# Kernel optimization log

Measured on AMD Instinct MI355X. Metric: run time of the kernel, lower is better.

Reference implementation:

```python
import jax, jax.numpy as jnp
import numpy as np

B = 64        # batch
V1 = 4096     # nodes, layer 1 (D)
V2 = 1024     # nodes after pool/4
DF = 8        # input features (DFeat)
K1 = 25       # Chebyshev order layer 1
K2 = 25       # Chebyshev order layer 2
F1 = 32       # CL1_F
F2 = 64       # CL2_F
FC1F = 512    # FC1_F
FC2F = 10     # FC2_F
E1 = 65536    # nnz of L1
E2 = 16384    # nnz of L2
FC1Fin = F2 * (V1 // 16)  # 16384


def setup_inputs() -> dict:
    key = jax.random.key(0)
    ks = jax.random.split(key, 16)
    x = jax.random.normal(ks[0], (B, V1, DF), jnp.float32)
    L1_rows = jax.random.randint(ks[1], (E1,), 0, V1, dtype=jnp.int32)
    L1_cols = jax.random.randint(ks[2], (E1,), 0, V1, dtype=jnp.int32)
    # small values keep the order-25 Chebyshev recursion numerically tame
    L1_vals = jax.random.normal(ks[3], (E1,), jnp.float32) * 0.05
    L2_rows = jax.random.randint(ks[4], (E2,), 0, V2, dtype=jnp.int32)
    L2_cols = jax.random.randint(ks[5], (E2,), 0, V2, dtype=jnp.int32)
    L2_vals = jax.random.normal(ks[6], (E2,), jnp.float32) * 0.05

    def glorot(k, shape, fin, fout):
        s = np.sqrt(2.0 / (fin + fout)).astype(np.float32)
        return jax.random.uniform(k, shape, jnp.float32, -s, s)

    cl1_w = glorot(ks[7], (F1, K1 * DF), K1, F1)
    cl1_b = jnp.zeros((F1,), jnp.float32)
    cl2_w = glorot(ks[8], (F2, K2 * F1), K2 * F1, F2)
    cl2_b = jnp.zeros((F2,), jnp.float32)
    fc1_w = glorot(ks[9], (FC1F, FC1Fin), FC1Fin, FC1F)
    fc1_b = jnp.zeros((FC1F,), jnp.float32)
    fc2_w = glorot(ks[10], (FC2F, FC1F), FC1F, FC2F)
    fc2_b = jnp.zeros((FC2F,), jnp.float32)
    return dict(x=x, L1_rows=L1_rows, L1_cols=L1_cols, L1_vals=L1_vals,
                L2_rows=L2_rows, L2_cols=L2_cols, L2_vals=L2_vals,
                cl1_w=cl1_w, cl1_b=cl1_b, cl2_w=cl2_w, cl2_b=cl2_b,
                fc1_w=fc1_w, fc1_b=fc1_b, fc2_w=fc2_w, fc2_b=fc2_b)


def _cheb_conv(x, rows, cols, vals, W, b, K):
    """Chebyshev graph conv. x: [B, V, Fin]; sparse L as COO edge lists."""
    Bb, V, Fin = x.shape
    x0 = x.transpose(1, 2, 0).reshape(V, Fin * Bb)  # [V, Fin*B]

    def spmm(y):  # sparse [V,V] @ dense [V, C]
        return jax.ops.segment_sum(vals[:, None] * y[cols], rows, num_segments=V)

    x1 = spmm(x0)

    def step(carry, _):
        xm2, xm1 = carry
        xk = 2.0 * spmm(xm1) - xm2
        return (xm1, xk), xk

    _, rest = jax.lax.scan(step, (x0, x1), None, length=K - 2)
    stack = jnp.concatenate([x0[None], x1[None], rest], axis=0)  # [K, V, Fin*B]
    # [K,V,Fin,B] -> [B,V,Fin,K] -> [B*V, Fin*K], matching torch layout
    feat = stack.reshape(K, V, Fin, Bb).transpose(3, 1, 2, 0).reshape(Bb * V, Fin * K)
    out = feat @ W.T + b
    return out.reshape(Bb, V, -1)


def _max_pool(x, p):
    Bb, V, F = x.shape
    return x.reshape(Bb, V // p, p, F).max(axis=2)


def reference(x, L1_rows, L1_cols, L1_vals, L2_rows, L2_cols, L2_vals,
              cl1_w, cl1_b, cl2_w, cl2_b, fc1_w, fc1_b, fc2_w, fc2_b):
    h = _cheb_conv(x, L1_rows, L1_cols, L1_vals, cl1_w, cl1_b, K1)
    h = jax.nn.relu(h)
    h = _max_pool(h, 4)                                   # [B, V/4, F1]
    h = _cheb_conv(h, L2_rows, L2_cols, L2_vals, cl2_w, cl2_b, K2)
    h = jax.nn.relu(h)
    h = _max_pool(h, 4)                                   # [B, V/16, F2]
    h = h.reshape(-1, FC1Fin)
    h = jax.nn.relu(h @ fc1_w.T + fc1_b)
    # dropout treated as identity (eval mode / d=0)
    return h @ fc2_w.T + fc2_b                            # [B, FC2F]
```

## Files before the change

kernel.cpp:

```cpp
#include <hip/hip_runtime.h>
#include <hip/hip_fp16.h>

#define B_    64
#define V1_   4096
#define V2_   1024
#define DF_   8
#define K_    25
#define NP_   13
#define F1_   32
#define F2_   64
#define FC1F_ 512
#define FC2F_ 10
#define E1_   65536
#define E2_   16384
#define C1_   512
#define C2_   2048
#define FCIN_ 16384

typedef short bf16x8 __attribute__((ext_vector_type(8)));
typedef float f32x4  __attribute__((ext_vector_type(4)));

#define FMA_MIX_LO(acc, qv, gv) \
    asm("v_fma_mix_f32 %0, %1, %2, %0 op_sel:[1,0,0] op_sel_hi:[1,1,0]" \
        : "+v"(acc) : "v"(qv), "v"(gv))
#define FMA_MIX_HI(acc, qv, gv) \
    asm("v_fma_mix_f32 %0, %1, %2, %0 op_sel:[1,1,0] op_sel_hi:[1,1,0]" \
        : "+v"(acc) : "v"(qv), "v"(gv))

__device__ __forceinline__ unsigned short f2bf(float x) {
    unsigned u = __float_as_uint(x);
    u += 0x7FFFu + ((u >> 16) & 1u);
    return (unsigned short)(u >> 16);
}
__device__ __forceinline__ float h2f_lo(unsigned u) {
    return __half2float(__ushort_as_half((unsigned short)(u & 0xFFFFu)));
}
__device__ __forceinline__ float h2f_hi(unsigned u) {
    return __half2float(__ushort_as_half((unsigned short)(u >> 16)));
}

__global__ __launch_bounds__(256) void k_transpose_rm(const float* __restrict__ x,
                                                      unsigned* __restrict__ XP,
                                                      unsigned* __restrict__ stk0) {
    __shared__ float tsh[DF_][B_][16];
    const int t = threadIdx.x;
    const int v0 = blockIdx.x * 16;
    for (int rep = 0; rep < 4; ++rep) {
        int idx = rep*256 + t;
        int b = idx >> 4, vv = idx & 15;
        const float4* p = (const float4*)&x[((size_t)b*V1_ + v0 + vv)*DF_];
        float4 a0 = p[0], a1 = p[1];
        tsh[0][b][vv]=a0.x; tsh[1][b][vv]=a0.y; tsh[2][b][vv]=a0.z; tsh[3][b][vv]=a0.w;
        tsh[4][b][vv]=a1.x; tsh[5][b][vv]=a1.y; tsh[6][b][vv]=a1.z; tsh[7][b][vv]=a1.w;
    }
    __syncthreads();
    for (int rep = 0; rep < 16; ++rep) {
        int idx = rep*256 + t;
        int c2 = idx & 255, vv = idx >> 8;
        int c = c2*2, fin = c >> 6, b = c & 63;
        float xa = tsh[fin][b][vv], xb = tsh[fin][b+1][vv];
        __half2 hh = __floats2half2_rn(xa, xb);
        XP[(size_t)(v0+vv)*256 + c2]   = *(const unsigned*)&hh;
        stk0[(size_t)(v0+vv)*256 + c2] = (unsigned)f2bf(xa) | ((unsigned)f2bf(xb) << 16);
    }
}

__global__ __launch_bounds__(256) void k_count(const int* __restrict__ rows, int E,
                                               int* __restrict__ cnt) {
    int e = blockIdx.x*256 + threadIdx.x;
    if (e < E) atomicAdd(&cnt[rows[e]], 1);
}

__global__ __launch_bounds__(256) void k_scan(const int* __restrict__ cnt, int V,
                                              int* __restrict__ offs, int* __restrict__ cursor) {
    __shared__ int psum[256];
    int t = threadIdx.x;
    int chunk = V >> 8;
    int lo = t*chunk;
    int s = 0;
    for (int i = lo; i < lo+chunk; ++i) s += (cnt[i] + 3) & ~3;
    psum[t] = s;
    __syncthreads();
    for (int off = 1; off < 256; off <<= 1) {
        int val = (t >= off) ? psum[t-off] : 0;
        __syncthreads();
        psum[t] += val;
        __syncthreads();
    }
    int run = (t == 0) ? 0 : psum[t-1];
    for (int i = lo; i < lo+chunk; ++i) {
        offs[i] = run; cursor[i] = run;
        run += (cnt[i] + 3) & ~3;
    }
    if (t == 255) offs[V] = run;
}

__global__ __launch_bounds__(256) void k_scatter(const int* __restrict__ rows,
                                                 const int* __restrict__ cols,
                                                 const float* __restrict__ vals, int E,
                                                 int shift,
                                                 int* __restrict__ cursor,
                                                 unsigned* __restrict__ ep) {
    int e = blockIdx.x*256 + threadIdx.x;
    if (e < E) {
        int p = atomicAdd(&cursor[rows[e]], 1);
        unsigned hv = (unsigned)__half_as_ushort(__float2half(vals[e]));
        ep[p] = (hv << 16) | ((unsigned)cols[e] << shift);
    }
}

__global__ __launch_bounds__(512) void k_dcheb1(int k,
        const unsigned short* __restrict__ Xsrc,
        unsigned short* __restrict__ Xown,
        unsigned short* __restrict__ stk16,
        const int* __restrict__ offs,
        const unsigned* __restrict__ ep) {
    const int t = threadIdx.x;
    const int lane = t & 63;
    const int v = blockIdx.x*8 + (t >> 6);
    const int e0 = offs[v], e1 = offs[v+1];
    const unsigned loff = (unsigned)lane * 16u;
    float acc[8];
#pragma unroll
    for (int j = 0; j < 8; ++j) acc[j] = 0.f;
    const char* srcb = (const char*)Xsrc;

    for (int e = e0; e < e1; e += 4) {
        const uint4 q = *(const uint4*)&ep[e];
        const uint4 g0 = *(const uint4*)(srcb + ((q.x & 0xFFFFu)*1024u + loff));
        const uint4 g1 = *(const uint4*)(srcb + ((q.y & 0xFFFFu)*1024u + loff));
        const uint4 g2 = *(const uint4*)(srcb + ((q.z & 0xFFFFu)*1024u + loff));
        const uint4 g3 = *(const uint4*)(srcb + ((q.w & 0xFFFFu)*1024u + loff));
        FMA_MIX_LO(acc[0], q.x, g0.x); FMA_MIX_HI(acc[1], q.x, g0.x);
        FMA_MIX_LO(acc[2], q.x, g0.y); FMA_MIX_HI(acc[3], q.x, g0.y);
        FMA_MIX_LO(acc[4], q.x, g0.z); FMA_MIX_HI(acc[5], q.x, g0.z);
        FMA_MIX_LO(acc[6], q.x, g0.w); FMA_MIX_HI(acc[7], q.x, g0.w);
        FMA_MIX_LO(acc[0], q.y, g1.x); FMA_MIX_HI(acc[1], q.y, g1.x);
        FMA_MIX_LO(acc[2], q.y, g1.y); FMA_MIX_HI(acc[3], q.y, g1.y);
        FMA_MIX_LO(acc[4], q.y, g1.z); FMA_MIX_HI(acc[5], q.y, g1.z);
        FMA_MIX_LO(acc[6], q.y, g1.w); FMA_MIX_HI(acc[7], q.y, g1.w);
        FMA_MIX_LO(acc[0], q.z, g2.x); FMA_MIX_HI(acc[1], q.z, g2.x);
        FMA_MIX_LO(acc[2], q.z, g2.y); FMA_MIX_HI(acc[3], q.z, g2.y);
        FMA_MIX_LO(acc[4], q.z, g2.z); FMA_MIX_HI(acc[5], q.z, g2.z);
        FMA_MIX_LO(acc[6], q.z, g2.w); FMA_MIX_HI(acc[7], q.z, g2.w);
        FMA_MIX_LO(acc[0], q.w, g3.x); FMA_MIX_HI(acc[1], q.w, g3.x);
        FMA_MIX_LO(acc[2], q.w, g3.y); FMA_MIX_HI(acc[3], q.w, g3.y);
        FMA_MIX_LO(acc[4], q.w, g3.z); FMA_MIX_HI(acc[5], q.w, g3.z);
        FMA_MIX_LO(acc[6], q.w, g3.w); FMA_MIX_HI(acc[7], q.w, g3.w);
    }

    float xn[8];
    if (k > 1) {
        const uint4 old = *(const uint4*)((const char*)Xown + ((size_t)v*1024 + loff));
        xn[0] = fmaf(2.f, acc[0], -h2f_lo(old.x));
        xn[1] = fmaf(2.f, acc[1], -h2f_hi(old.x));
        xn[2] = fmaf(2.f, acc[2], -h2f_lo(old.y));
        xn[3] = fmaf(2.f, acc[3], -h2f_hi(old.y));
        xn[4] = fmaf(2.f, acc[4], -h2f_lo(old.z));
        xn[5] = fmaf(2.f, acc[5], -h2f_hi(old.z));
        xn[6] = fmaf(2.f, acc[6], -h2f_lo(old.w));
        xn[7] = fmaf(2.f, acc[7], -h2f_hi(old.w));
    } else {
#pragma unroll
        for (int j = 0; j < 8; ++j) xn[j] = acc[j];
    }

    uint4 hp;
    { __half2 h0 = __floats2half2_rn(xn[0], xn[1]); hp.x = *(const unsigned*)&h0;
      __half2 h1 = __floats2half2_rn(xn[2], xn[3]); hp.y = *(const unsigned*)&h1;
      __half2 h2 = __floats2half2_rn(xn[4], xn[5]); hp.z = *(const unsigned*)&h2;
      __half2 h3 = __floats2half2_rn(xn[6], xn[7]); hp.w = *(const unsigned*)&h3; }
    *(uint4*)((char*)Xown + ((size_t)v*1024 + loff)) = hp;

    uint4 bp;
    bp.x = (unsigned)f2bf(xn[0]) | ((unsigned)f2bf(xn[1]) << 16);
    bp.y = (unsigned)f2bf(xn[2]) | ((unsigned)f2bf(xn[3]) << 16);
    bp.z = (unsigned)f2bf(xn[4]) | ((unsigned)f2bf(xn[5]) << 16);
    bp.w = (unsigned)f2bf(xn[6]) | ((unsigned)f2bf(xn[7]) << 16);
    *(uint4*)((char*)stk16 + (((size_t)k*V1_ + v)*1024 + loff)) = bp;
}

template<int FIN, int F>
__global__ __launch_bounds__(256) void k_wprep(const float* __restrict__ W,
                                               unsigned short* __restrict__ Wb) {
    int idx = blockIdx.x*256 + threadIdx.x;
    int kk  = idx & 7;
    int f   = (idx >> 3) % F;
    int g   = (idx >> 3) / F % 4;
    int fin = idx / (8*F*4);
    int k = g*8 + kk;
    Wb[idx] = (k < K_) ? f2bf(W[(size_t)f*(FIN*K_) + fin*K_ + k]) : 0;
}

__global__ __launch_bounds__(256) void k_wprep_fc(const float* __restrict__ W,
                                                  unsigned short* __restrict__ Wb) {
    int idx = (blockIdx.x*256 + threadIdx.x)*4;
    float4 w = *(const float4*)&W[idx];
    ushort4 o;
    o.x = f2bf(w.x); o.y = f2bf(w.y); o.z = f2bf(w.z); o.w = f2bf(w.w);
    *(ushort4*)&Wb[idx] = o;
}

__global__ __launch_bounds__(256) void k_gemm1b(const unsigned short* __restrict__ stk16,
                                                const unsigned short* __restrict__ Wb,
                                                const float* __restrict__ bias,
                                                float* __restrict__ X0T2) {
    const int t = threadIdx.x, lane = t & 63, wave = t >> 6;
    const int v2 = blockIdx.x*4 + wave;
    const int m = lane & 15, g = lane >> 4;
    int kbase[8];
#pragma unroll
    for (int j = 0; j < 8; ++j) {
        int kq = g*8 + j; if (kq > 24) kq = 24;
        kbase[j] = kq * (V1_*C1_);
    }
    float bv[2] = { bias[m], bias[16+m] };
    f32x4 pool[4][2];

    for (int vv = 0; vv < 4; ++vv) {
        const int v = v2*4 + vv;
        f32x4 acc[4][2];
#pragma unroll
        for (int mt = 0; mt < 4; ++mt)
#pragma unroll
            for (int ft = 0; ft < 2; ++ft) acc[mt][ft] = (f32x4){0.f,0.f,0.f,0.f};

        for (int fin = 0; fin < DF_; ++fin) {
            const int cbase = v*C1_ + fin*64 + m;
            const bf16x8 bw0 = *(const bf16x8*)&Wb[((fin*4+g)*F1_ + m)*8];
            const bf16x8 bw1 = *(const bf16x8*)&Wb[((fin*4+g)*F1_ + 16 + m)*8];
#pragma unroll
            for (int mt = 0; mt < 4; ++mt) {
                unsigned short au[8];
#pragma unroll
                for (int j = 0; j < 8; ++j)
                    au[j] = stk16[(size_t)(kbase[j] + cbase + mt*16)];
                bf16x8 a;
                __builtin_memcpy(&a, au, 16);
                acc[mt][0] = __builtin_amdgcn_mfma_f32_16x16x32_bf16(a, bw0, acc[mt][0], 0,0,0);
                acc[mt][1] = __builtin_amdgcn_mfma_f32_16x16x32_bf16(a, bw1, acc[mt][1], 0,0,0);
            }
        }
#pragma unroll
        for (int mt = 0; mt < 4; ++mt)
#pragma unroll
            for (int ft = 0; ft < 2; ++ft) {
                if (vv == 0) pool[mt][ft] = acc[mt][ft];
                else {
#pragma unroll
                    for (int j = 0; j < 4; ++j)
                        pool[mt][ft][j] = fmaxf(pool[mt][ft][j], acc[mt][ft][j]);
                }
            }
    }

#pragma unroll
    for (int mt = 0; mt < 4; ++mt)
#pragma unroll
        for (int ft = 0; ft < 2; ++ft)
#pragma unroll
            for (int j = 0; j < 4; ++j) {
                float mx = fmaxf(pool[mt][ft][j] + bv[ft], 0.f);
                int b = mt*16 + g*4 + j;
                int f = ft*16 + m;
                X0T2[(size_t)(f*64+b)*V2_ + v2] = mx;
            }
}

template<int V, int THREADS, int MINW>
__global__ __launch_bounds__(THREADS, MINW) void k_cheb2(
        const float* __restrict__ X0T,
        const int* __restrict__ offs,
        const unsigned* __restrict__ ep,
        unsigned* __restrict__ stk) {
    constexpr int RPT = V / THREADS;
    __shared__ uint2 buf[2*V];
    const int c0 = blockIdx.x*4;
    const int t = threadIdx.x;
    int e0r[RPT], e1r[RPT];
    unsigned tlo[RPT][4];
    unsigned* __restrict__ pl[4];
#pragma unroll
    for (int j = 0; j < 4; ++j) pl[j] = stk + (size_t)(c0+j)*NP_*V;

#pragma unroll
    for (int r = 0; r < RPT; ++r) {
        const int v = r*THREADS + t;
        e0r[r] = offs[v]; e1r[r] = offs[v+1];
        float xj[4];
#pragma unroll
        for (int j = 0; j < 4; ++j) {
            xj[j] = X0T[(size_t)(c0+j)*V + v];
            tlo[r][j] = f2bf(xj[j]);
        }
        __half2 ha = __floats2half2_rn(xj[0], xj[1]);
        __half2 hb = __floats2half2_rn(xj[2], xj[3]);
        buf[v] = make_uint2(*(const unsigned*)&ha, *(const unsigned*)&hb);
    }
    __syncthreads();

    auto step = [&](const uint2* __restrict__ src, uint2* __restrict__ dst,
                    bool first, bool last, int plane) {
#pragma unroll
        for (int r = 0; r < RPT; ++r) {
            const int v = r*THREADS + t;
            float acc[4][4];
#pragma unroll
            for (int j = 0; j < 4; ++j)
#pragma unroll
                for (int i = 0; i < 4; ++i) acc[j][i] = 0.f;
            const int ee0 = e0r[r], ee1 = e1r[r];
            uint4 q = *(const uint4*)&ep[ee0];
            for (int e = ee0; e < ee1; e += 4) {
                const uint4 qn = *(const uint4*)&ep[e + 4];
                const uint2 g0 = *(const uint2*)((const char*)src + (q.x & 0xFFFFu));
                const uint2 g1 = *(const uint2*)((const char*)src + (q.y & 0xFFFFu));
                const uint2 g2 = *(const uint2*)((const char*)src + (q.z & 0xFFFFu));
                const uint2 g3 = *(const uint2*)((const char*)src + (q.w & 0xFFFFu));
                FMA_MIX_LO(acc[0][0], q.x, g0.x); FMA_MIX_HI(acc[1][0], q.x, g0.x);
                FMA_MIX_LO(acc[2][0], q.x, g0.y); FMA_MIX_HI(acc[3][0], q.x, g0.y);
                FMA_MIX_LO(acc[0][1], q.y, g1.x); FMA_MIX_HI(acc[1][1], q.y, g1.x);
                FMA_MIX_LO(acc[2][1], q.y, g1.y); FMA_MIX_HI(acc[3][1], q.y, g1.y);
                FMA_MIX_LO(acc[0][2], q.z, g2.x); FMA_MIX_HI(acc[1][2], q.z, g2.x);
                FMA_MIX_LO(acc[2][2], q.z, g2.y); FMA_MIX_HI(acc[3][2], q.z, g2.y);
                FMA_MIX_LO(acc[0][3], q.w, g3.x); FMA_MIX_HI(acc[1][3], q.w, g3.x);
                FMA_MIX_LO(acc[2][3], q.w, g3.y); FMA_MIX_HI(acc[3][3], q.w, g3.y);
                q = qn;
            }
            float gs[4];
#pragma unroll
            for (int j = 0; j < 4; ++j)
                gs[j] = (acc[j][0]+acc[j][1])+(acc[j][2]+acc[j][3]);
            float xn[4];
            if (first) {
#pragma unroll
                for (int j = 0; j < 4; ++j) xn[j] = gs[j];
            } else {
                const uint2 old = dst[v];
                xn[0] = fmaf(2.f, gs[0], -h2f_lo(old.x));
                xn[1] = fmaf(2.f, gs[1], -h2f_hi(old.x));
                xn[2] = fmaf(2.f, gs[2], -h2f_lo(old.y));
                xn[3] = fmaf(2.f, gs[3], -h2f_hi(old.y));
            }
            if (!last) {
                __half2 ha = __floats2half2_rn(xn[0], xn[1]);
                __half2 hb = __floats2half2_rn(xn[2], xn[3]);
                dst[v] = make_uint2(*(const unsigned*)&ha, *(const unsigned*)&hb);
            }
            unsigned h[4];
#pragma unroll
            for (int j = 0; j < 4; ++j) h[j] = f2bf(xn[j]);
            if (plane < 0) {
#pragma unroll
                for (int j = 0; j < 4; ++j) tlo[r][j] = h[j];
            } else {
#pragma unroll
                for (int j = 0; j < 4; ++j)
                    pl[j][(size_t)plane*V + v] = tlo[r][j] | (h[j] << 16);
            }
        }
        __syncthreads();
    };

    step(buf, buf + V, true, false, 0);
    for (int k = 2; k < 24; k += 2) {
        step(buf + V, buf, false, false, -1);
        step(buf, buf + V, false, false, (k + 1) >> 1);
    }
    step(buf + V, buf, false, true, -1);

#pragma unroll
    for (int r = 0; r < RPT; ++r) {
        const int v = r*THREADS + t;
#pragma unroll
        for (int j = 0; j < 4; ++j)
            pl[j][(size_t)12*V + v] = tlo[r][j];
    }
}

__global__ __launch_bounds__(256) void k_gemm2(const unsigned* __restrict__ STK,
                                               const unsigned short* __restrict__ Wb,
                                               const float* __restrict__ bias,
                                               unsigned short* __restrict__ ABF) {
    const int t = threadIdx.x, lane = t & 63, wave = t >> 6;
    const int b = blockIdx.x;
    const int v0 = blockIdx.y*128 + wave*32;
    const int m = lane & 15, g = lane >> 4;
    int offp[4];
#pragma unroll
    for (int p = 0; p < 4; ++p) {
        int pl = 4*g + p; if (pl > 12) pl = 12;
        offp[p] = pl*V2_ + v0 + m;
    }

    f32x4 acc[2][4];
#pragma unroll
    for (int mt = 0; mt < 2; ++mt)
#pragma unroll
        for (int ft = 0; ft < 4; ++ft) acc[mt][ft] = (f32x4){0.f,0.f,0.f,0.f};

#pragma unroll 4
    for (int fin = 0; fin < F1_; ++fin) {
        const unsigned* sp = STK + (size_t)(fin*64 + b)*(NP_*V2_);
        unsigned ua[4], ub[4];
#pragma unroll
        for (int p = 0; p < 4; ++p) { ua[p] = sp[offp[p]]; ub[p] = sp[offp[p] + 16]; }
        bf16x8 a0, a1;
        __builtin_memcpy(&a0, ua, 16);
        __builtin_memcpy(&a1, ub, 16);
#pragma unroll
        for (int ft = 0; ft < 4; ++ft) {
            const bf16x8 bw = *(const bf16x8*)&Wb[((fin*4+g)*F2_ + ft*16 + m)*8];
            acc[0][ft] = __builtin_amdgcn_mfma_f32_16x16x32_bf16(a0, bw, acc[0][ft], 0,0,0);
            acc[1][ft] = __builtin_amdgcn_mfma_f32_16x16x32_bf16(a1, bw, acc[1][ft], 0,0,0);
        }
    }
#pragma unroll
    for (int mt = 0; mt < 2; ++mt)
#pragma unroll
        for (int ft = 0; ft < 4; ++ft) {
            f32x4 a = acc[mt][ft];
            float mx = fmaxf(fmaxf(a[0],a[1]), fmaxf(a[2],a[3])) + bias[ft*16 + m];
            mx = fmaxf(mx, 0.f);
            int v2 = blockIdx.y*32 + wave*8 + mt*4 + g;
            ABF[(size_t)b*FCIN_ + v2*64 + ft*16 + m] = f2bf(mx);
        }
}

__global__ __launch_bounds__(256) void k_fc1_init(const float* __restrict__ bias,
                                                  float* __restrict__ O) {
    int idx = blockIdx.x*256 + threadIdx.x;
    O[idx] = bias[idx & (FC1F_-1)];
}

__global__ __launch_bounds__(256) void k_fc1m(const unsigned short* __restrict__ ABF,
                                              const unsigned short* __restrict__ WBF,
                                              float* __restrict__ O) {
    const int t = threadIdx.x, lane = t & 63, wave = t >> 6;
    const int j0 = blockIdx.x*16;
    const int k0 = blockIdx.y*1024;
    const int m = lane & 15, g = lane >> 4;
    const int m0 = wave*16;
    f32x4 acc = (f32x4){0.f,0.f,0.f,0.f};
#pragma unroll 4
    for (int k = k0; k < k0+1024; k += 32) {
        const bf16x8 a = *(const bf16x8*)&ABF[(size_t)(m0+m)*FCIN_ + k + g*8];
        const bf16x8 w = *(const bf16x8*)&WBF[(size_t)(j0+m)*FCIN_ + k + g*8];
        acc = __builtin_amdgcn_mfma_f32_16x16x32_bf16(a, w, acc, 0,0,0);
    }
#pragma unroll
    for (int r = 0; r < 4; ++r)
        atomicAdd(&O[(size_t)(m0 + g*4 + r)*FC1F_ + j0 + m], acc[r]);
}

__global__ void k_fc2(const float* __restrict__ O1, const float* __restrict__ W2,
                      const float* __restrict__ b2, float* __restrict__ out) {
    int c = blockIdx.x;
    int b = threadIdx.x;
    float s = b2[c];
    for (int j = 0; j < FC1F_; ++j)
        s = fmaf(fmaxf(O1[b*FC1F_ + j], 0.f), W2[c*FC1F_ + j], s);
    out[b*FC2F_ + c] = s;
}

extern "C" void kernel_launch(void* const* d_in, const int* in_sizes, int n_in,
                              void* d_out, int out_size, void* d_ws, size_t ws_size,
                              hipStream_t stream) {
    const float* x   = (const float*)d_in[0];
    const int*   l1r = (const int*)d_in[1];
    const int*   l1c = (const int*)d_in[2];
    const float* l1v = (const float*)d_in[3];
    const int*   l2r = (const int*)d_in[4];
    const int*   l2c = (const int*)d_in[5];
    const float* l2v = (const float*)d_in[6];
    const float* w1  = (const float*)d_in[7];
    const float* b1  = (const float*)d_in[8];
    const float* w2  = (const float*)d_in[9];
    const float* b2  = (const float*)d_in[10];
    const float* fw1 = (const float*)d_in[11];
    const float* fb1 = (const float*)d_in[12];
    const float* fw2 = (const float*)d_in[13];
    const float* fb2 = (const float*)d_in[14];
    float* out = (float*)d_out;

    char* wsp = (char*)d_ws;
    size_t off = 0;
    auto alloc = [&](size_t bytes) -> void* {
        void* p = wsp + off;
        off += (bytes + 255) & ~size_t(255);
        return p;
    };
    void*     STKU  = alloc((size_t)C2_*NP_*V2_*4);
    unsigned short* stk16 = (unsigned short*)STKU;
    unsigned*       STACK = (unsigned*)STKU;
    unsigned short* XB0   = (unsigned short*)alloc((size_t)V1_*C1_*2);
    unsigned short* XB1   = (unsigned short*)alloc((size_t)V1_*C1_*2);
    float*    X0T2  = (float*)alloc((size_t)C2_*V2_*4);
    unsigned short* ABF = (unsigned short*)alloc((size_t)B_*FCIN_*2);
    unsigned short* WBF = (unsigned short*)alloc((size_t)FC1F_*FCIN_*2);
    float*    FC1O  = (float*)alloc((size_t)B_*FC1F_*4);
    unsigned short* WB1 = (unsigned short*)alloc((size_t)DF_*4*F1_*8*2);
    unsigned short* WB2 = (unsigned short*)alloc((size_t)F1_*4*F2_*8*2);
    int*      cnt1  = (int*)alloc(V1_*4);
    int*      offs1 = (int*)alloc((V1_+1)*4);
    int*      cur1  = (int*)alloc(V1_*4);
    unsigned* ep1   = (unsigned*)alloc((size_t)(E1_ + 4*V1_ + 8)*4);
    int*      cnt2  = (int*)alloc(V2_*4);
    int*      offs2 = (int*)alloc((V2_+1)*4);
    int*      cur2  = (int*)alloc(V2_*4);
    unsigned* ep2   = (unsigned*)alloc((size_t)(E2_ + 4*V2_ + 8)*4);

    hipMemsetAsync(cnt1, 0, V1_*4, stream);
    hipMemsetAsync(ep1, 0, (size_t)(E1_ + 4*V1_ + 8)*4, stream);
    hipMemsetAsync(cnt2, 0, V2_*4, stream);
    hipMemsetAsync(ep2, 0, (size_t)(E2_ + 4*V2_ + 8)*4, stream);
    hipLaunchKernelGGL(k_count,   dim3(E1_/256), dim3(256), 0, stream, l1r, E1_, cnt1);
    hipLaunchKernelGGL(k_scan,    dim3(1),       dim3(256), 0, stream, cnt1, V1_, offs1, cur1);
    hipLaunchKernelGGL(k_scatter, dim3(E1_/256), dim3(256), 0, stream, l1r, l1c, l1v, E1_, 0, cur1, ep1);
    hipLaunchKernelGGL(k_count,   dim3(E2_/256), dim3(256), 0, stream, l2r, E2_, cnt2);
    hipLaunchKernelGGL(k_scan,    dim3(1),       dim3(256), 0, stream, cnt2, V2_, offs2, cur2);
    hipLaunchKernelGGL(k_scatter, dim3(E2_/256), dim3(256), 0, stream, l2r, l2c, l2v, E2_, 3, cur2, ep2);
    hipLaunchKernelGGL((k_wprep<DF_,F1_>), dim3(DF_*4*F1_*8/256), dim3(256), 0, stream, w1, WB1);
    hipLaunchKernelGGL((k_wprep<F1_,F2_>), dim3(F1_*4*F2_*8/256), dim3(256), 0, stream, w2, WB2);
    hipLaunchKernelGGL(k_wprep_fc, dim3(FC1F_*FCIN_/1024), dim3(256), 0, stream, fw1, WBF);

    hipLaunchKernelGGL(k_transpose_rm, dim3(V1_/16), dim3(256), 0, stream,
                       x, (unsigned*)XB0, (unsigned*)stk16);
    for (int k = 1; k <= 24; ++k) {
        unsigned short* src = (k & 1) ? XB0 : XB1;
        unsigned short* own = (k & 1) ? XB1 : XB0;
        hipLaunchKernelGGL(k_dcheb1, dim3(V1_/8), dim3(512), 0, stream,
                           k, src, own, stk16, offs1, ep1);
    }
    hipLaunchKernelGGL(k_gemm1b, dim3(V2_/4), dim3(256), 0, stream, stk16, WB1, b1, X0T2);

    hipLaunchKernelGGL((k_cheb2<V2_,512,4>), dim3(C2_/4), dim3(512), 0, stream,
                       X0T2, offs2, ep2, STACK);
    hipLaunchKernelGGL(k_gemm2, dim3(64, 8), dim3(256), 0, stream, STACK, WB2, b2, ABF);

    hipLaunchKernelGGL(k_fc1_init, dim3(B_*FC1F_/256), dim3(256), 0, stream, fb1, FC1O);
    hipLaunchKernelGGL(k_fc1m, dim3(32, 16), dim3(256), 0, stream, ABF, WBF, FC1O);
    hipLaunchKernelGGL(k_fc2, dim3(FC2F_), dim3(B_), 0, stream, FC1O, fw2, fb2, out);
}
```

Baseline: 520.8 us.

## Pack Chebyshev stack as bf16 pairs, split nodes across two waves, use nontemporal stores

The layer-1 Chebyshev stack is now written as interleaved bf16 pairs (k even/odd) only on odd steps, so the GEMM can load 32-bit words instead of gathering 16-bit scalars across eight planes. Each node is now handled by two waves with half-width loads, doubling the block size to 1024 threads. Nontemporal loads and stores are added across several kernels to reduce cache pollution, and the cheb2 launch changes to 1024 threads with a different template parameter. The costs are an extra reread of the source row on odd steps and a changed register and occupancy profile.

```diff
diff --git a/kernel.cpp b/kernel.cpp
--- a/kernel.cpp
+++ b/kernel.cpp
@@ -19,6 +19,8 @@
 
 typedef short bf16x8 __attribute__((ext_vector_type(8)));
 typedef float f32x4  __attribute__((ext_vector_type(4)));
+typedef unsigned u32x2 __attribute__((ext_vector_type(2)));
+typedef unsigned u32x4 __attribute__((ext_vector_type(4)));
 
 #define FMA_MIX_LO(acc, qv, gv) \
     asm("v_fma_mix_f32 %0, %1, %2, %0 op_sel:[1,0,0] op_sel_hi:[1,1,0]" \
@@ -40,8 +42,7 @@
 }
 
 __global__ __launch_bounds__(256) void k_transpose_rm(const float* __restrict__ x,
-                                                      unsigned* __restrict__ XP,
-                                                      unsigned* __restrict__ stk0) {
+                                                      unsigned* __restrict__ XP) {
     __shared__ float tsh[DF_][B_][16];
     const int t = threadIdx.x;
     const int v0 = blockIdx.x * 16;
@@ -58,10 +59,9 @@
         int idx = rep*256 + t;
         int c2 = idx & 255, vv = idx >> 8;
         int c = c2*2, fin = c >> 6, b = c & 63;
-        float xa = tsh[fin][b][vv], xb = tsh[fin][b+1][vv];
-        __half2 hh = __floats2half2_rn(xa, xb);
-        XP[(size_t)(v0+vv)*256 + c2]   = *(const unsigned*)&hh;
-        stk0[(size_t)(v0+vv)*256 + c2] = (unsigned)f2bf(xa) | ((unsigned)f2bf(xb) << 16);
+        __half2 hh = __floats2half2_rn(tsh[fin][b][vv], tsh[fin][b+1][vv]);
+        __builtin_nontemporal_store(*(const unsigned*)&hh,
+                                    &XP[(size_t)(v0+vv)*256 + c2]);
     }
 }
 
@@ -109,75 +109,74 @@
     }
 }
 
-__global__ __launch_bounds__(512) void k_dcheb1(int k,
+__global__ __launch_bounds__(1024, 8) void k_dcheb1(int k,
         const unsigned short* __restrict__ Xsrc,
         unsigned short* __restrict__ Xown,
-        unsigned short* __restrict__ stk16,
+        unsigned* __restrict__ ppstk,
         const int* __restrict__ offs,
         const unsigned* __restrict__ ep) {
     const int t = threadIdx.x;
     const int lane = t & 63;
-    const int v = blockIdx.x*8 + (t >> 6);
+    const int v = blockIdx.x*8 + (t >> 7);
+    const int h = (t >> 6) & 1;
     const int e0 = offs[v], e1 = offs[v+1];
-    const unsigned loff = (unsigned)lane * 16u;
-    float acc[8];
-#pragma unroll
-    for (int j = 0; j < 8; ++j) acc[j] = 0.f;
+    const unsigned coff = (unsigned)h*512u + (unsigned)lane*8u;
+    float acc[4] = {0.f, 0.f, 0.f, 0.f};
     const char* srcb = (const char*)Xsrc;
 
     for (int e = e0; e < e1; e += 4) {
         const uint4 q = *(const uint4*)&ep[e];
-        const uint4 g0 = *(const uint4*)(srcb + ((q.x & 0xFFFFu)*1024u + loff));
-        const uint4 g1 = *(const uint4*)(srcb + ((q.y & 0xFFFFu)*1024u + loff));
-        const uint4 g2 = *(const uint4*)(srcb + ((q.z & 0xFFFFu)*1024u + loff));
-        const uint4 g3 = *(const uint4*)(srcb + ((q.w & 0xFFFFu)*1024u + loff));
+        const uint2 g0 = *(const uint2*)(srcb + ((q.x & 0xFFFFu)*1024u + coff));
+        const uint2 g1 = *(const uint2*)(srcb + ((q.y & 0xFFFFu)*1024u + coff));
+        const uint2 g2 = *(const uint2*)(srcb + ((q.z & 0xFFFFu)*1024u + coff));
+        const uint2 g3 = *(const uint2*)(srcb + ((q.w & 0xFFFFu)*1024u + coff));
         FMA_MIX_LO(acc[0], q.x, g0.x); FMA_MIX_HI(acc[1], q.x, g0.x);
         FMA_MIX_LO(acc[2], q.x, g0.y); FMA_MIX_HI(acc[3], q.x, g0.y);
-        FMA_MIX_LO(acc[4], q.x, g0.z); FMA_MIX_HI(acc[5], q.x, g0.z);
-        FMA_MIX_LO(acc[6], q.x, g0.w); FMA_MIX_HI(acc[7], q.x, g0.w);
         FMA_MIX_LO(acc[0], q.y, g1.x); FMA_MIX_HI(acc[1], q.y, g1.x);
         FMA_MIX_LO(acc[2], q.y, g1.y); FMA_MIX_HI(acc[3], q.y, g1.y);
-        FMA_MIX_LO(acc[4], q.y, g1.z); FMA_MIX_HI(acc[5], q.y, g1.z);
-        FMA_MIX_LO(acc[6], q.y, g1.w); FMA_MIX_HI(acc[7], q.y, g1.w);
         FMA_MIX_LO(acc[0], q.z, g2.x); FMA_MIX_HI(acc[1], q.z, g2.x);
         FMA_MIX_LO(acc[2], q.z, g2.y); FMA_MIX_HI(acc[3], q.z, g2.y);
-        FMA_MIX_LO(acc[4], q.z, g2.z); FMA_MIX_HI(acc[5], q.z, g2.z);
-        FMA_MIX_LO(acc[6], q.z, g2.w); FMA_MIX_HI(acc[7], q.z, g2.w);
         FMA_MIX_LO(acc[0], q.w, g3.x); FMA_MIX_HI(acc[1], q.w, g3.x);
         FMA_MIX_LO(acc[2], q.w, g3.y); FMA_MIX_HI(acc[3], q.w, g3.y);
-        FMA_MIX_LO(acc[4], q.w, g3.z); FMA_MIX_HI(acc[5], q.w, g3.z);
-        FMA_MIX_LO(acc[6], q.w, g3.w); FMA_MIX_HI(acc[7], q.w, g3.w);
-    }
-
-    float xn[8];
+    }
+
+    float xn[4];
     if (k > 1) {
-        const uint4 old = *(const uint4*)((const char*)Xown + ((size_t)v*1024 + loff));
+        const uint2 old = *(const uint2*)((const char*)Xown + ((size_t)v*1024 + coff));
         xn[0] = fmaf(2.f, acc[0], -h2f_lo(old.x));
         xn[1] = fmaf(2.f, acc[1], -h2f_hi(old.x));
         xn[2] = fmaf(2.f, acc[2], -h2f_lo(old.y));
         xn[3] = fmaf(2.f, acc[3], -h2f_hi(old.y));
-        xn[4] = fmaf(2.f, acc[4], -h2f_lo(old.z));
-        xn[5] = fmaf(2.f, acc[5], -h2f_hi(old.z));
-        xn[6] = fmaf(2.f, acc[6], -h2f_lo(old.w));
-        xn[7] = fmaf(2.f, acc[7], -h2f_hi(old.w));
     } else {
 #pragma unroll
-        for (int j = 0; j < 8; ++j) xn[j] = acc[j];
-    }
-
-    uint4 hp;
-    { __half2 h0 = __floats2half2_rn(xn[0], xn[1]); hp.x = *(const unsigned*)&h0;
-      __half2 h1 = __floats2half2_rn(xn[2], xn[3]); hp.y = *(const unsigned*)&h1;
-      __half2 h2 = __floats2half2_rn(xn[4], xn[5]); hp.z = *(const unsigned*)&h2;
-      __half2 h3 = __floats2half2_rn(xn[6], xn[7]); hp.w = *(const unsigned*)&h3; }
-    *(uint4*)((char*)Xown + ((size_t)v*1024 + loff)) = hp;
-
-    uint4 bp;
-    bp.x = (unsigned)f2bf(xn[0]) | ((unsigned)f2bf(xn[1]) << 16);
-    bp.y = (unsigned)f2bf(xn[2]) | ((unsigned)f2bf(xn[3]) << 16);
-    bp.z = (unsigned)f2bf(xn[4]) | ((unsigned)f2bf(xn[5]) << 16);
-    bp.w = (unsigned)f2bf(xn[6]) | ((unsigned)f2bf(xn[7]) << 16);
-    *(uint4*)((char*)stk16 + (((size_t)k*V1_ + v)*1024 + loff)) = bp;
+        for (int j = 0; j < 4; ++j) xn[j] = acc[j];
+    }
+
+    {
+        __half2 ha = __floats2half2_rn(xn[0], xn[1]);
+        __half2 hb = __floats2half2_rn(xn[2], xn[3]);
+        u32x2 hp = { *(const unsigned*)&ha, *(const unsigned*)&hb };
+        __builtin_nontemporal_store(hp,
+            (u32x2*)((char*)Xown + ((size_t)v*1024 + coff)));
+    }
+
+    if (k & 1) {
+        const uint2 own = *(const uint2*)(srcb + ((size_t)v*1024 + coff));
+        const int p = k >> 1;
+        u32x4 pr;
+        pr.x = (unsigned)f2bf(h2f_lo(own.x)) | ((unsigned)f2bf(xn[0]) << 16);
+        pr.y = (unsigned)f2bf(h2f_hi(own.x)) | ((unsigned)f2bf(xn[1]) << 16);
+        pr.z = (unsigned)f2bf(h2f_lo(own.y)) | ((unsigned)f2bf(xn[2]) << 16);
+        pr.w = (unsigned)f2bf(h2f_hi(own.y)) | ((unsigned)f2bf(xn[3]) << 16);
+        __builtin_nontemporal_store(pr,
+            (u32x4*)&ppstk[((size_t)p*V1_ + v)*512 + h*256 + lane*4]);
+    } else if (k == 24) {
+        u32x4 pr;
+        pr.x = f2bf(xn[0]); pr.y = f2bf(xn[1]);
+        pr.z = f2bf(xn[2]); pr.w = f2bf(xn[3]);
+        __builtin_nontemporal_store(pr,
+            (u32x4*)&ppstk[((size_t)12*V1_ + v)*512 + h*256 + lane*4]);
+    }
 }
 
 template<int FIN, int F>
@@ -201,18 +200,18 @@
     *(ushort4*)&Wb[idx] = o;
 }
 
-__global__ __launch_bounds__(256) void k_gemm1b(const unsigned short* __restrict__ stk16,
+__global__ __launch_bounds__(256) void k_gemm1c(const unsigned* __restrict__ pp,
                                                 const unsigned short* __restrict__ Wb,
                                                 const float* __restrict__ bias,
                                                 float* __restrict__ X0T2) {
     const int t = threadIdx.x, lane = t & 63, wave = t >> 6;
     const int v2 = blockIdx.x*4 + wave;
     const int m = lane & 15, g = lane >> 4;
-    int kbase[8];
-#pragma unroll
-    for (int j = 0; j < 8; ++j) {
-        int kq = g*8 + j; if (kq > 24) kq = 24;
-        kbase[j] = kq * (V1_*C1_);
+    size_t pbase[4];
+#pragma unroll
+    for (int p = 0; p < 4; ++p) {
+        int pq = g*4 + p; if (pq > 12) pq = 12;
+        pbase[p] = (size_t)pq * V1_ * 512;
     }
     float bv[2] = { bias[m], bias[16+m] };
     f32x4 pool[4][2];
@@ -226,17 +225,17 @@
             for (int ft = 0; ft < 2; ++ft) acc[mt][ft] = (f32x4){0.f,0.f,0.f,0.f};
 
         for (int fin = 0; fin < DF_; ++fin) {
-            const int cbase = v*C1_ + fin*64 + m;
+            const int cbase = v*512 + fin*64 + m;
             const bf16x8 bw0 = *(const bf16x8*)&Wb[((fin*4+g)*F1_ + m)*8];
             const bf16x8 bw1 = *(const bf16x8*)&Wb[((fin*4+g)*F1_ + 16 + m)*8];
 #pragma unroll
             for (int mt = 0; mt < 4; ++mt) {
-                unsigned short au[8];
-#pragma unroll
-                for (int j = 0; j < 8; ++j)
-                    au[j] = stk16[(size_t)(kbase[j] + cbase + mt*16)];
+                unsigned ua[4];
+#pragma unroll
+                for (int p = 0; p < 4; ++p)
+                    ua[p] = __builtin_nontemporal_load(&pp[pbase[p] + cbase + mt*16]);
                 bf16x8 a;
-                __builtin_memcpy(&a, au, 16);
+                __builtin_memcpy(&a, ua, 16);
                 acc[mt][0] = __builtin_amdgcn_mfma_f32_16x16x32_bf16(a, bw0, acc[mt][0], 0,0,0);
                 acc[mt][1] = __builtin_amdgcn_mfma_f32_16x16x32_bf16(a, bw1, acc[mt][1], 0,0,0);
             }
@@ -356,7 +355,8 @@
             } else {
 #pragma unroll
                 for (int j = 0; j < 4; ++j)
-                    pl[j][(size_t)plane*V + v] = tlo[r][j] | (h[j] << 16);
+                    __builtin_nontemporal_store(tlo[r][j] | (h[j] << 16),
+                        &pl[j][(size_t)plane*V + v]);
             }
         }
         __syncthreads();
@@ -374,7 +374,7 @@
         const int v = r*THREADS + t;
 #pragma unroll
         for (int j = 0; j < 4; ++j)
-            pl[j][(size_t)12*V + v] = tlo[r][j];
+            __builtin_nontemporal_store(tlo[r][j], &pl[j][(size_t)12*V + v]);
     }
 }
 
@@ -404,7 +404,10 @@
         const unsigned* sp = STK + (size_t)(fin*64 + b)*(NP_*V2_);
         unsigned ua[4], ub[4];
 #pragma unroll
-        for (int p = 0; p < 4; ++p) { ua[p] = sp[offp[p]]; ub[p] = sp[offp[p] + 16]; }
+        for (int p = 0; p < 4; ++p) {
+            ua[p] = __builtin_nontemporal_load(&sp[offp[p]]);
+            ub[p] = __builtin_nontemporal_load(&sp[offp[p] + 16]);
+        }
         bf16x8 a0, a1;
         __builtin_memcpy(&a0, ua, 16);
         __builtin_memcpy(&a1, ub, 16);
@@ -445,7 +448,10 @@
 #pragma unroll 4
     for (int k = k0; k < k0+1024; k += 32) {
         const bf16x8 a = *(const bf16x8*)&ABF[(size_t)(m0+m)*FCIN_ + k + g*8];
-        const bf16x8 w = *(const bf16x8*)&WBF[(size_t)(j0+m)*FCIN_ + k + g*8];
+        u32x4 wr = __builtin_nontemporal_load(
+            (const u32x4*)&WBF[(size_t)(j0+m)*FCIN_ + k + g*8]);
+        bf16x8 w;
+        __builtin_memcpy(&w, &wr, 16);
         acc = __builtin_amdgcn_mfma_f32_16x16x32_bf16(a, w, acc, 0,0,0);
     }
 #pragma unroll
@@ -491,8 +497,8 @@
         return p;
     };
     void*     STKU  = alloc((size_t)C2_*NP_*V2_*4);
-    unsigned short* stk16 = (unsigned short*)STKU;
-    unsigned*       STACK = (unsigned*)STKU;
+    unsigned* ppstk = (unsigned*)STKU;
+    unsigned* STACK = (unsigned*)STKU;
     unsigned short* XB0   = (unsigned short*)alloc((size_t)V1_*C1_*2);
     unsigned short* XB1   = (unsigned short*)alloc((size_t)V1_*C1_*2);
     float*    X0T2  = (float*)alloc((size_t)C2_*V2_*4);
@@ -524,17 +530,16 @@
     hipLaunchKernelGGL((k_wprep<F1_,F2_>), dim3(F1_*4*F2_*8/256), dim3(256), 0, stream, w2, WB2);
     hipLaunchKernelGGL(k_wprep_fc, dim3(FC1F_*FCIN_/1024), dim3(256), 0, stream, fw1, WBF);
 
-    hipLaunchKernelGGL(k_transpose_rm, dim3(V1_/16), dim3(256), 0, stream,
-                       x, (unsigned*)XB0, (unsigned*)stk16);
+    hipLaunchKernelGGL(k_transpose_rm, dim3(V1_/16), dim3(256), 0, stream, x, (unsigned*)XB0);
     for (int k = 1; k <= 24; ++k) {
         unsigned short* src = (k & 1) ? XB0 : XB1;
         unsigned short* own = (k & 1) ? XB1 : XB0;
-        hipLaunchKernelGGL(k_dcheb1, dim3(V1_/8), dim3(512), 0, stream,
-                           k, src, own, stk16, offs1, ep1);
-    }
-    hipLaunchKernelGGL(k_gemm1b, dim3(V2_/4), dim3(256), 0, stream, stk16, WB1, b1, X0T2);
-
-    hipLaunchKernelGGL((k_cheb2<V2_,512,4>), dim3(C2_/4), dim3(512), 0, stream,
+        hipLaunchKernelGGL(k_dcheb1, dim3(V1_/8), dim3(1024), 0, stream,
+                           k, src, own, ppstk, offs1, ep1);
+    }
+    hipLaunchKernelGGL(k_gemm1c, dim3(V2_/4), dim3(256), 0, stream, ppstk, WB1, b1, X0T2);
+
+    hipLaunchKernelGGL((k_cheb2<V2_,1024,8>), dim3(C2_/4), dim3(1024), 0, stream,
                        X0T2, offs2, ep2, STACK);
     hipLaunchKernelGGL(k_gemm2, dim3(64, 8), dim3(256), 0, stream, STACK, WB2, b2, ABF);
 
```

Measured after the change: 574.5 us. +10.3%, slower.
